# Kernel tuning notes

Hardware: AMD Instinct MI355X
Metric: run time of the kernel (lower is better)

## Reference

```python
import jax, jax.numpy as jnp
import numpy as np

N = 100_000
E = 1_600_000
IN_FT, HID, OUT = 512, 128, 64


def setup_inputs() -> dict:
    key = jax.random.key(0)
    ks = jax.random.split(key, 7)
    x = jax.random.normal(ks[0], (N, IN_FT), dtype=jnp.float32)
    edge_index = jax.random.randint(ks[1], (2, E), 0, N, dtype=jnp.int32)
    edge_weight = jax.random.uniform(ks[2], (E,), dtype=jnp.float32)
    W1 = jax.random.normal(ks[3], (IN_FT, HID), dtype=jnp.float32) * 0.05
    b1 = jnp.zeros((HID,), dtype=jnp.float32)
    W2 = jax.random.normal(ks[4], (HID, OUT), dtype=jnp.float32) * 0.05
    b2 = jnp.zeros((OUT,), dtype=jnp.float32)
    return {"x": x, "edge_index": edge_index, "edge_weight": edge_weight,
            "W1": W1, "b1": b1, "W2": W2, "b2": b2}


def reference(x, edge_index, edge_weight, W1, b1, W2, b2):
    n = x.shape[0]
    row, col = edge_index[0], edge_index[1]
    # PyG gcn_norm: add self-loops with weight 1, symmetric normalization
    loop = jnp.arange(n, dtype=row.dtype)
    r = jnp.concatenate([row, loop])
    c = jnp.concatenate([col, loop])
    w = jnp.concatenate([edge_weight, jnp.ones((n,), edge_weight.dtype)])
    deg = jax.ops.segment_sum(w, c, num_segments=n)
    dinv = jnp.where(deg > 0, jax.lax.rsqrt(deg), 0.0)
    norm = dinv[r] * w * dinv[c]  # [E + N]

    def conv(h, W, b):
        h = h @ W                                  # [N, F_out]
        msg = norm[:, None] * h[r]                 # gather source nodes
        return jax.ops.segment_sum(msg, c, num_segments=n) + b

    h = jax.nn.relu(conv(x, W1, b1))
    # dropout: inference mode (training=False) -> identity
    out = conv(h, W2, b2)
    return jax.nn.log_softmax(out, axis=1)
```

## Files before the change

kernel.cpp:

```cpp
#include <hip/hip_runtime.h>
#include <hip/hip_fp16.h>


constexpr int NN  = 100000;
constexpr int NE  = 1600000;
constexpr int FIN = 512;
constexpr int FH  = 128;
constexpr int FO  = 64;
constexpr int CAP = 64;

constexpr int NBLK1 = 512;
constexpr int EPB   = NE / NBLK1;
constexpr int NBKT  = 196;
constexpr int BCAP  = 9728;
constexpr int NWT   = FIN * FH + FH * FO;

constexpr float WSCALE  = 32767.0f;
constexpr float IWSCALE = 1.0f / 32767.0f;

typedef _Float16 f16x8 __attribute__((ext_vector_type(8)));
typedef float    f32x4 __attribute__((ext_vector_type(4)));

union F16Frag { _Float16 f[8]; short4 s[2]; f16x8 v; };

__device__ __forceinline__ void gload16(const void* g, void* l) {
    __builtin_amdgcn_global_load_lds(
        (const __attribute__((address_space(1))) void*)g,
        (__attribute__((address_space(3))) void*)l,
        16, 0, 0);
}


__global__ __launch_bounds__(256) void k_pass1(const int* __restrict__ rowi,
                                               const int* __restrict__ coli,
                                               const float* __restrict__ ew,
                                               const float* __restrict__ W1,
                                               const float* __restrict__ W2,
                                               _Float16* __restrict__ w1t,
                                               _Float16* __restrict__ w2t,
                                               int* __restrict__ bcur,
                                               unsigned long long* __restrict__ binned) {
    __shared__ unsigned long long buf[EPB];
    __shared__ int hist[NBKT];
    __shared__ int curs[NBKT];
    const int t = threadIdx.x;
    {
        int i = blockIdx.x * 256 + t;
        if (i < FIN * FH) {
            int k = i >> 7, c = i & 127;
            w1t[c * FIN + k] = (_Float16)W1[i];
        } else if (i < NWT) {
            int j = i - FIN * FH;
            int k = j >> 6, c = j & 63;
            w2t[c * FH + k] = (_Float16)W2[j];
        }
    }
    const int base = blockIdx.x * EPB;
    for (int i = t; i < NBKT; i += 256) hist[i] = 0;
    __syncthreads();
    for (int i = t; i < EPB; i += 256) {
        int e = base + i;
        int c = coli[e];
        unsigned wq = __float2uint_rn(ew[e] * WSCALE);
        buf[i] = ((unsigned long long)(unsigned)c << 32)
               | (unsigned long long)((wq << 17) | (unsigned)rowi[e]);
        atomicAdd(&hist[c >> 9], 1);
    }
    __syncthreads();
    if (t < NBKT) curs[t] = atomicAdd(&bcur[t], hist[t]);
    __syncthreads();
    for (int i = t; i < EPB; i += 256) {
        unsigned long long v = buf[i];
        int b = (int)(v >> 41);
        int pos = atomicAdd(&curs[b], 1);
        if ((unsigned)pos < BCAP) binned[(size_t)b * BCAP + pos] = v;
    }
}


__global__ __launch_bounds__(256) void k_pass2(const int* __restrict__ bcur,
                                               const unsigned long long* __restrict__ binned,
                                               unsigned* __restrict__ pay,
                                               int* __restrict__ cursor,
                                               float* __restrict__ dinv) {
    __shared__ int   cnt[512];
    __shared__ float wsum[512];
    const int t = threadIdx.x, b = blockIdx.x;
    for (int i = t; i < 512; i += 256) { cnt[i] = 0; wsum[i] = 0.f; }
    __syncthreads();
    const int total = min(bcur[b], BCAP);
    const int nbase = b * 512;
    for (int i = t; i < total; i += 256) {
        unsigned long long v = binned[(size_t)b * BCAP + i];
        int c9 = (int)((v >> 32) & 511);
        unsigned lo = (unsigned)v;
        int pos = atomicAdd(&cnt[c9], 1);
        atomicAdd(&wsum[c9], (float)(lo >> 17) * IWSCALE);
        if (pos < CAP) pay[(size_t)(nbase + c9) * CAP + pos] = lo;
    }
    __syncthreads();
    for (int i = t; i < 512; i += 256) {
        int node = nbase + i;
        if (node < NN) {
            cursor[node] = cnt[i];
            dinv[node]   = rsqrtf(1.0f + wsum[i]);
        }
    }
}


__global__ __launch_bounds__(256) void k_gemm1(const float* __restrict__ X,
                                               const _Float16* __restrict__ w1t,
                                               _Float16* __restrict__ H1) {
    __shared__ __align__(16) float    Asf[128 * 64];
    __shared__ __align__(16) _Float16 Bs[128 * 64];
    const int tid = threadIdx.x;
    const int wid = tid >> 6, l = tid & 63;
    const int wr = wid >> 1, wc = wid & 1;
    const int l15 = l & 15, lg = l >> 4;
    const int brow = blockIdx.x * 128;

    f32x4 acc[4][4];
#pragma unroll
    for (int m = 0; m < 4; ++m)
#pragma unroll
        for (int n = 0; n < 4; ++n) acc[m][n] = (f32x4){0.f, 0.f, 0.f, 0.f};

    const int rA = wid * 32 + (l >> 4);
    const int sA = l & 15;
    const int rB = wid * 32 + (l >> 3);
    const int sB = l & 7;

    for (int k0 = 0; k0 < FIN; k0 += 64) {
#pragma unroll
        for (int j = 0; j < 8; ++j) {
            int r  = rA + j * 4;
            int sg = sA ^ (r & 15);
            gload16(&X[(size_t)min(brow + r, NN - 1) * FIN + k0 + sg * 4],
                    &Asf[wid * 2048 + j * 256]);
        }
#pragma unroll
        for (int j = 0; j < 4; ++j) {
            int r  = rB + j * 8;
            int sg = sB ^ (r & 7);
            gload16(&w1t[(size_t)r * FIN + k0 + sg * 8],
                    &Bs[wid * 2048 + j * 512]);
        }
        __syncthreads();
#pragma unroll
        for (int ks = 0; ks < 2; ++ks) {
            F16Frag au[4], bu[4];
#pragma unroll
            for (int m = 0; m < 4; ++m) {
                int row = wr * 64 + m * 16 + l15;
                int slo = ks * 8 + lg;
                float4 lo = *(const float4*)&Asf[row * 64 + ((slo       ^ (row & 15)) * 4)];
                float4 hi = *(const float4*)&Asf[row * 64 + (((slo + 4) ^ (row & 15)) * 4)];
                au[m].f[0] = (_Float16)lo.x; au[m].f[1] = (_Float16)lo.y;
                au[m].f[2] = (_Float16)lo.z; au[m].f[3] = (_Float16)lo.w;
                au[m].f[4] = (_Float16)hi.x; au[m].f[5] = (_Float16)hi.y;
                au[m].f[6] = (_Float16)hi.z; au[m].f[7] = (_Float16)hi.w;
            }
#pragma unroll
            for (int n = 0; n < 4; ++n) {
                int row = wc * 64 + n * 16 + l15;
                int sb  = ks * 4 + (lg >> 1);
                int wi  = (lg & 1) * 4;
                bu[n].s[0] = *(const short4*)&Bs[row * 64 + ((sb       ^ (row & 7)) * 8) + wi];
                bu[n].s[1] = *(const short4*)&Bs[row * 64 + (((sb + 2) ^ (row & 7)) * 8) + wi];
            }
#pragma unroll
            for (int m = 0; m < 4; ++m)
#pragma unroll
                for (int n = 0; n < 4; ++n)
                    acc[m][n] = __builtin_amdgcn_mfma_f32_16x16x32_f16(
                        au[m].v, bu[n].v, acc[m][n], 0, 0, 0);
        }
        __syncthreads();
    }
#pragma unroll
    for (int m = 0; m < 4; ++m)
#pragma unroll
        for (int n = 0; n < 4; ++n) {
            int gcol = wc * 64 + n * 16 + l15;
#pragma unroll
            for (int r4 = 0; r4 < 4; ++r4) {
                int gr = brow + wr * 64 + m * 16 + lg * 4 + r4;
                if (gr < NN) H1[(size_t)gr * FH + gcol] = (_Float16)acc[m][n][r4];
            }
        }
}


__global__ __launch_bounds__(256) void k_gemm2(const _Float16* __restrict__ H2,
                                               const _Float16* __restrict__ w2t,
                                               _Float16* __restrict__ H3) {
    __shared__ __align__(16) _Float16 As[64 * 128];
    __shared__ __align__(16) _Float16 Bs[64 * 128];
    const int tid  = threadIdx.x;
    const int brow = blockIdx.x * 64;
    const int wid = tid >> 6, l = tid & 63;
    const int wr = wid >> 1, wc = wid & 1;
    const int l15 = l & 15, lg = l >> 4;

    f32x4 acc[2][2];
#pragma unroll
    for (int m = 0; m < 2; ++m)
#pragma unroll
        for (int n = 0; n < 2; ++n) acc[m][n] = (f32x4){0.f, 0.f, 0.f, 0.f};

    {
        int ar = tid >> 2, part = tid & 3, grow = brow + ar;
#pragma unroll
        for (int j = 0; j < 4; ++j) {
            int slot = part * 4 + j;
            int4 v = make_int4(0, 0, 0, 0);
            if (grow < NN) v = *(const int4*)&H2[(size_t)grow * FH + slot * 8];
            *(int4*)&As[ar * 128 + ((slot ^ (ar & 15)) * 8)] = v;
            *(int4*)&Bs[ar * 128 + ((slot ^ (ar & 15)) * 8)] =
                *(const int4*)&w2t[ar * FH + slot * 8];
        }
    }
    __syncthreads();
#pragma unroll
    for (int ks = 0; ks < 4; ++ks) {
        F16Frag au[2], bu[2];
        int klo = ks * 32 + 4 * lg;
        int khi = klo + 16;
#pragma unroll
        for (int m = 0; m < 2; ++m) {
            int row = wr * 32 + m * 16 + l15;
            int sw  = row & 15;
            au[m].s[0] = *(const short4*)&As[row * 128 + (((klo >> 3) ^ sw) * 8) + (klo & 7)];
            au[m].s[1] = *(const short4*)&As[row * 128 + (((khi >> 3) ^ sw) * 8) + (khi & 7)];
        }
#pragma unroll
        for (int n = 0; n < 2; ++n) {
            int row = wc * 32 + n * 16 + l15;
            int sw  = row & 15;
            bu[n].s[0] = *(const short4*)&Bs[row * 128 + (((klo >> 3) ^ sw) * 8) + (klo & 7)];
            bu[n].s[1] = *(const short4*)&Bs[row * 128 + (((khi >> 3) ^ sw) * 8) + (khi & 7)];
        }
#pragma unroll
        for (int m = 0; m < 2; ++m)
#pragma unroll
            for (int n = 0; n < 2; ++n)
                acc[m][n] = __builtin_amdgcn_mfma_f32_16x16x32_f16(
                    au[m].v, bu[n].v, acc[m][n], 0, 0, 0);
    }
#pragma unroll
    for (int m = 0; m < 2; ++m)
#pragma unroll
        for (int n = 0; n < 2; ++n) {
            int gcol = wc * 32 + n * 16 + l15;
#pragma unroll
            for (int r4 = 0; r4 < 4; ++r4) {
                int gr = brow + wr * 32 + m * 16 + lg * 4 + r4;
                if (gr < NN) H3[(size_t)gr * FO + gcol] = (_Float16)acc[m][n][r4];
            }
        }
}


__global__ __launch_bounds__(256) void k_agg1(const int* __restrict__ cursor,
                                              const unsigned* __restrict__ pay,
                                              const float* __restrict__ dinv,
                                              const __half* __restrict__ H1,
                                              const float* __restrict__ b1,
                                              __half* __restrict__ H2) {
    int node = (blockIdx.x * 256 + threadIdx.x) >> 6;
    int lane = threadIdx.x & 63;
    if (node >= NN) return;
    const int f = lane * 2;
    float dc  = dinv[node];
    float dcs = dc * IWSCALE;
    float2 hc = __half22float2(*(const __half2*)&H1[(size_t)node * FH + f]);
    float a0x = dc * dc * hc.x, a0y = dc * dc * hc.y;
    float a1x = 0, a1y = 0, a2x = 0, a2y = 0, a3x = 0, a3y = 0;
    int cnt = min(max(cursor[node], 0), CAP);
    const unsigned* p = &pay[(size_t)node * CAP];
    int e = 0;
    for (; e + 8 <= cnt; e += 8) {
        uint4 pa = *(const uint4*)&p[e];
        uint4 pb = *(const uint4*)&p[e + 4];
        int s0 = pa.x & 0x1FFFF, s1 = pa.y & 0x1FFFF, s2 = pa.z & 0x1FFFF, s3 = pa.w & 0x1FFFF;
        int s4 = pb.x & 0x1FFFF, s5 = pb.y & 0x1FFFF, s6 = pb.z & 0x1FFFF, s7 = pb.w & 0x1FFFF;
        float w0 = (float)(pa.x >> 17) * dcs * dinv[s0];
        float w1 = (float)(pa.y >> 17) * dcs * dinv[s1];
        float w2 = (float)(pa.z >> 17) * dcs * dinv[s2];
        float w3 = (float)(pa.w >> 17) * dcs * dinv[s3];
        float w4 = (float)(pb.x >> 17) * dcs * dinv[s4];
        float w5 = (float)(pb.y >> 17) * dcs * dinv[s5];
        float w6 = (float)(pb.z >> 17) * dcs * dinv[s6];
        float w7 = (float)(pb.w >> 17) * dcs * dinv[s7];
        float2 g0 = __half22float2(*(const __half2*)&H1[(size_t)s0 * FH + f]);
        float2 g1 = __half22float2(*(const __half2*)&H1[(size_t)s1 * FH + f]);
        float2 g2 = __half22float2(*(const __half2*)&H1[(size_t)s2 * FH + f]);
        float2 g3 = __half22float2(*(const __half2*)&H1[(size_t)s3 * FH + f]);
        float2 g4 = __half22float2(*(const __half2*)&H1[(size_t)s4 * FH + f]);
        float2 g5 = __half22float2(*(const __half2*)&H1[(size_t)s5 * FH + f]);
        float2 g6 = __half22float2(*(const __half2*)&H1[(size_t)s6 * FH + f]);
        float2 g7 = __half22float2(*(const __half2*)&H1[(size_t)s7 * FH + f]);
        a0x += w0 * g0.x; a0y += w0 * g0.y;  a1x += w1 * g1.x; a1y += w1 * g1.y;
        a2x += w2 * g2.x; a2y += w2 * g2.y;  a3x += w3 * g3.x; a3y += w3 * g3.y;
        a0x += w4 * g4.x; a0y += w4 * g4.y;  a1x += w5 * g5.x; a1y += w5 * g5.y;
        a2x += w6 * g6.x; a2y += w6 * g6.y;  a3x += w7 * g7.x; a3y += w7 * g7.y;
    }
    for (; e < cnt; ++e) {
        unsigned v = p[e];
        int s = v & 0x1FFFF;
        float w = (float)(v >> 17) * dcs * dinv[s];
        float2 g = __half22float2(*(const __half2*)&H1[(size_t)s * FH + f]);
        a0x += w * g.x; a0y += w * g.y;
    }
    float vx = a0x + a1x + a2x + a3x + b1[f];
    float vy = a0y + a1y + a2y + a3y + b1[f + 1];
    vx = vx > 0.f ? vx : 0.f;
    vy = vy > 0.f ? vy : 0.f;
    *(__half2*)&H2[(size_t)node * FH + f] = __floats2half2_rn(vx, vy);
}


__global__ __launch_bounds__(256) void k_agg2(const int* __restrict__ cursor,
                                              const unsigned* __restrict__ pay,
                                              const float* __restrict__ dinv,
                                              const __half* __restrict__ H3,
                                              const float* __restrict__ b2,
                                              float* __restrict__ out) {
    int node = (blockIdx.x * 256 + threadIdx.x) >> 6;
    int lane = threadIdx.x & 63;
    if (node >= NN) return;
    float dc  = dinv[node];
    float dcs = dc * IWSCALE;
    float a0 = dc * dc * __half2float(H3[(size_t)node * FO + lane]);
    float a1 = 0, a2 = 0, a3 = 0;
    int cnt = min(max(cursor[node], 0), CAP);
    const unsigned* p = &pay[(size_t)node * CAP];
    int e = 0;
    for (; e + 8 <= cnt; e += 8) {
        uint4 pa = *(const uint4*)&p[e];
        uint4 pb = *(const uint4*)&p[e + 4];
        int s0 = pa.x & 0x1FFFF, s1 = pa.y & 0x1FFFF, s2 = pa.z & 0x1FFFF, s3 = pa.w & 0x1FFFF;
        int s4 = pb.x & 0x1FFFF, s5 = pb.y & 0x1FFFF, s6 = pb.z & 0x1FFFF, s7 = pb.w & 0x1FFFF;
        float w0 = (float)(pa.x >> 17) * dcs * dinv[s0];
        float w1 = (float)(pa.y >> 17) * dcs * dinv[s1];
        float w2 = (float)(pa.z >> 17) * dcs * dinv[s2];
        float w3 = (float)(pa.w >> 17) * dcs * dinv[s3];
        float w4 = (float)(pb.x >> 17) * dcs * dinv[s4];
        float w5 = (float)(pb.y >> 17) * dcs * dinv[s5];
        float w6 = (float)(pb.z >> 17) * dcs * dinv[s6];
        float w7 = (float)(pb.w >> 17) * dcs * dinv[s7];
        a0 += w0 * __half2float(H3[(size_t)s0 * FO + lane]);
        a1 += w1 * __half2float(H3[(size_t)s1 * FO + lane]);
        a2 += w2 * __half2float(H3[(size_t)s2 * FO + lane]);
        a3 += w3 * __half2float(H3[(size_t)s3 * FO + lane]);
        a0 += w4 * __half2float(H3[(size_t)s4 * FO + lane]);
        a1 += w5 * __half2float(H3[(size_t)s5 * FO + lane]);
        a2 += w6 * __half2float(H3[(size_t)s6 * FO + lane]);
        a3 += w7 * __half2float(H3[(size_t)s7 * FO + lane]);
    }
    for (; e < cnt; ++e) {
        unsigned v = p[e];
        int s = v & 0x1FFFF;
        float w = (float)(v >> 17) * dcs * dinv[s];
        a0 += w * __half2float(H3[(size_t)s * FO + lane]);
    }
    float v = a0 + a1 + a2 + a3 + b2[lane];
    float m = v;
#pragma unroll
    for (int s = 32; s; s >>= 1) m = fmaxf(m, __shfl_xor(m, s));
    float ex = expf(v - m);
    float sum = ex;
#pragma unroll
    for (int s = 32; s; s >>= 1) sum += __shfl_xor(sum, s);
    out[(size_t)node * FO + lane] = v - m - logf(sum);
}


extern "C" void kernel_launch(void* const* d_in, const int* in_sizes, int n_in,
                              void* d_out, int out_size, void* d_ws, size_t ws_size,
                              hipStream_t stream) {
    const float* x   = (const float*)d_in[0];
    const int*   ei  = (const int*)d_in[1];
    const int*   row = ei;
    const int*   col = ei + NE;
    const float* ew  = (const float*)d_in[2];
    const float* W1  = (const float*)d_in[3];
    const float* b1  = (const float*)d_in[4];
    const float* W2  = (const float*)d_in[5];
    const float* b2  = (const float*)d_in[6];
    float* out = (float*)d_out;

    int*       bcur   = (int*)d_ws;
    int*       cursor = bcur + 256;
    float*     dinv   = (float*)(cursor + 102400);
    _Float16*  w1t    = (_Float16*)(dinv + 102400);
    _Float16*  w2t    = w1t + FIN * FH;
    unsigned long long* binned = (unsigned long long*)(w2t + FH * FO);
    unsigned*  pay    = (unsigned*)(binned + (size_t)NBKT * BCAP);
    _Float16*  H1     = (_Float16*)(pay + (size_t)NN * CAP);
    _Float16*  H2     = H1 + (size_t)NN * FH;
    _Float16*  H3     = H2 + (size_t)NN * FH;

    hipMemsetAsync(bcur, 0, NBKT * sizeof(int), stream);
    k_pass1<<<NBLK1, 256, 0, stream>>>(row, col, ew, W1, W2, w1t, w2t, bcur, binned);
    k_pass2<<<NBKT, 256, 0, stream>>>(bcur, binned, pay, cursor, dinv);

    k_gemm1<<<(NN + 127) / 128, 256, 0, stream>>>(x, w1t, H1);
    k_agg1 <<<(NN * 64 + 255) / 256, 256, 0, stream>>>(cursor, pay, dinv,
                                                       (const __half*)H1, b1, (__half*)H2);
    k_gemm2<<<(NN + 63) / 64, 256, 0, stream>>>(H2, w2t, H3);
    k_agg2 <<<(NN * 64 + 255) / 256, 256, 0, stream>>>(cursor, pay, dinv,
                                                       (const __half*)H3, b2, out);
}
```

Baseline: 260.5 us.

## Merge edge binning into the first GEMM launch and fold memset into prep

The edge-binning pass and the first feature GEMM are merged into one launch. The extra blocks at the end of the grid do the binning, and the earlier blocks run the GEMM, with shared memory overlaid through a union. Weight conversion and zeroing of the bucket counters move into a small prep kernel, which replaces the memset. The aim is to overlap the memory-bound binning with the GEMM and to drop launch gaps. The cost is that every block now reserves the larger shared footprint (buf is 25KB versus 48KB for the GEMM, so 48KB), and the extra prep launch must finish first.

```diff
diff --git a/kernel.cpp b/kernel.cpp
--- a/kernel.cpp
+++ b/kernel.cpp
@@ -14,6 +14,7 @@
 constexpr int NBKT  = 196;
 constexpr int BCAP  = 9728;
 constexpr int NWT   = FIN * FH + FH * FO;
+constexpr int NG    = (NN + 127) / 128;
 
 constexpr float WSCALE  = 32767.0f;
 constexpr float IWSCALE = 1.0f / 32767.0f;
@@ -31,50 +32,146 @@
 }
 
 
-__global__ __launch_bounds__(256) void k_pass1(const int* __restrict__ rowi,
-                                               const int* __restrict__ coli,
-                                               const float* __restrict__ ew,
-                                               const float* __restrict__ W1,
-                                               const float* __restrict__ W2,
-                                               _Float16* __restrict__ w1t,
-                                               _Float16* __restrict__ w2t,
-                                               int* __restrict__ bcur,
-                                               unsigned long long* __restrict__ binned) {
-    __shared__ unsigned long long buf[EPB];
-    __shared__ int hist[NBKT];
-    __shared__ int curs[NBKT];
-    const int t = threadIdx.x;
-    {
-        int i = blockIdx.x * 256 + t;
-        if (i < FIN * FH) {
-            int k = i >> 7, c = i & 127;
-            w1t[c * FIN + k] = (_Float16)W1[i];
-        } else if (i < NWT) {
-            int j = i - FIN * FH;
-            int k = j >> 6, c = j & 63;
-            w2t[c * FH + k] = (_Float16)W2[j];
-        }
-    }
-    const int base = blockIdx.x * EPB;
-    for (int i = t; i < NBKT; i += 256) hist[i] = 0;
-    __syncthreads();
-    for (int i = t; i < EPB; i += 256) {
-        int e = base + i;
-        int c = coli[e];
-        unsigned wq = __float2uint_rn(ew[e] * WSCALE);
-        buf[i] = ((unsigned long long)(unsigned)c << 32)
-               | (unsigned long long)((wq << 17) | (unsigned)rowi[e]);
-        atomicAdd(&hist[c >> 9], 1);
-    }
-    __syncthreads();
-    if (t < NBKT) curs[t] = atomicAdd(&bcur[t], hist[t]);
-    __syncthreads();
-    for (int i = t; i < EPB; i += 256) {
-        unsigned long long v = buf[i];
-        int b = (int)(v >> 41);
-        int pos = atomicAdd(&curs[b], 1);
-        if ((unsigned)pos < BCAP) binned[(size_t)b * BCAP + pos] = v;
-    }
+__global__ __launch_bounds__(256) void k_prep(const float* __restrict__ W1,
+                                              const float* __restrict__ W2,
+                                              int* __restrict__ bcur,
+                                              _Float16* __restrict__ w1t,
+                                              _Float16* __restrict__ w2t) {
+    int i = blockIdx.x * 256 + threadIdx.x;
+    if (i < NBKT) bcur[i] = 0;
+    if (i < FIN * FH) {
+        int k = i >> 7, c = i & 127;
+        w1t[c * FIN + k] = (_Float16)W1[i];
+    } else if (i < NWT) {
+        int j = i - FIN * FH;
+        int k = j >> 6, c = j & 63;
+        w2t[c * FH + k] = (_Float16)W2[j];
+    }
+}
+
+
+union MegaShared {
+    struct {
+        float    Asf[128 * 64];
+        _Float16 Bs[128 * 64];
+    } g;
+    struct {
+        unsigned long long buf[EPB];
+        int hist[NBKT];
+        int curs[NBKT];
+    } b;
+};
+
+__global__ __launch_bounds__(256) void k_mega(const float* __restrict__ X,
+                                              const _Float16* __restrict__ w1t,
+                                              _Float16* __restrict__ H1,
+                                              const int* __restrict__ rowi,
+                                              const int* __restrict__ coli,
+                                              const float* __restrict__ ew,
+                                              int* __restrict__ bcur,
+                                              unsigned long long* __restrict__ binned) {
+    __shared__ MegaShared sm;
+    const int tid = threadIdx.x;
+
+    if (blockIdx.x >= NG) {
+        const int bb   = blockIdx.x - NG;
+        const int base = bb * EPB;
+        for (int i = tid; i < NBKT; i += 256) sm.b.hist[i] = 0;
+        __syncthreads();
+        for (int i = tid; i < EPB; i += 256) {
+            int e = base + i;
+            int c = coli[e];
+            unsigned wq = __float2uint_rn(ew[e] * WSCALE);
+            sm.b.buf[i] = ((unsigned long long)(unsigned)c << 32)
+                        | (unsigned long long)((wq << 17) | (unsigned)rowi[e]);
+            atomicAdd(&sm.b.hist[c >> 9], 1);
+        }
+        __syncthreads();
+        if (tid < NBKT) sm.b.curs[tid] = atomicAdd(&bcur[tid], sm.b.hist[tid]);
+        __syncthreads();
+        for (int i = tid; i < EPB; i += 256) {
+            unsigned long long v = sm.b.buf[i];
+            int b = (int)(v >> 41);
+            int pos = atomicAdd(&sm.b.curs[b], 1);
+            if ((unsigned)pos < BCAP) binned[(size_t)b * BCAP + pos] = v;
+        }
+        return;
+    }
+
+    const int wid = tid >> 6, l = tid & 63;
+    const int wr = wid >> 1, wc = wid & 1;
+    const int l15 = l & 15, lg = l >> 4;
+    const int brow = blockIdx.x * 128;
+
+    f32x4 acc[4][4];
+#pragma unroll
+    for (int m = 0; m < 4; ++m)
+#pragma unroll
+        for (int n = 0; n < 4; ++n) acc[m][n] = (f32x4){0.f, 0.f, 0.f, 0.f};
+
+    const int rA = wid * 32 + (l >> 4);
+    const int sA = l & 15;
+    const int rB = wid * 32 + (l >> 3);
+    const int sB = l & 7;
+
+    for (int k0 = 0; k0 < FIN; k0 += 64) {
+#pragma unroll
+        for (int j = 0; j < 8; ++j) {
+            int r  = rA + j * 4;
+            int sg = sA ^ (r & 15);
+            gload16(&X[(size_t)min(brow + r, NN - 1) * FIN + k0 + sg * 4],
+                    &sm.g.Asf[wid * 2048 + j * 256]);
+        }
+#pragma unroll
+        for (int j = 0; j < 4; ++j) {
+            int r  = rB + j * 8;
+            int sg = sB ^ (r & 7);
+            gload16(&w1t[(size_t)r * FIN + k0 + sg * 8],
+                    &sm.g.Bs[wid * 2048 + j * 512]);
+        }
+        __syncthreads();
+#pragma unroll
+        for (int ks = 0; ks < 2; ++ks) {
+            F16Frag au[4], bu[4];
+#pragma unroll
+            for (int m = 0; m < 4; ++m) {
+                int row = wr * 64 + m * 16 + l15;
+                int slo = ks * 8 + lg;
+                float4 lo = *(const float4*)&sm.g.Asf[row * 64 + ((slo       ^ (row & 15)) * 4)];
+                float4 hi = *(const float4*)&sm.g.Asf[row * 64 + (((slo + 4) ^ (row & 15)) * 4)];
+                au[m].f[0] = (_Float16)lo.x; au[m].f[1] = (_Float16)lo.y;
+                au[m].f[2] = (_Float16)lo.z; au[m].f[3] = (_Float16)lo.w;
+                au[m].f[4] = (_Float16)hi.x; au[m].f[5] = (_Float16)hi.y;
+                au[m].f[6] = (_Float16)hi.z; au[m].f[7] = (_Float16)hi.w;
+            }
+#pragma unroll
+            for (int n = 0; n < 4; ++n) {
+                int row = wc * 64 + n * 16 + l15;
+                int sb  = ks * 4 + (lg >> 1);
+                int wi  = (lg & 1) * 4;
+                bu[n].s[0] = *(const short4*)&sm.g.Bs[row * 64 + ((sb       ^ (row & 7)) * 8) + wi];
+                bu[n].s[1] = *(const short4*)&sm.g.Bs[row * 64 + (((sb + 2) ^ (row & 7)) * 8) + wi];
+            }
+#pragma unroll
+            for (int m = 0; m < 4; ++m)
+#pragma unroll
+                for (int n = 0; n < 4; ++n)
+                    acc[m][n] = __builtin_amdgcn_mfma_f32_16x16x32_f16(
+                        au[m].v, bu[n].v, acc[m][n], 0, 0, 0);
+        }
+        __syncthreads();
+    }
+#pragma unroll
+    for (int m = 0; m < 4; ++m)
+#pragma unroll
+        for (int n = 0; n < 4; ++n) {
+            int gcol = wc * 64 + n * 16 + l15;
+#pragma unroll
+            for (int r4 = 0; r4 < 4; ++r4) {
+                int gr = brow + wr * 64 + m * 16 + lg * 4 + r4;
+                if (gr < NN) H1[(size_t)gr * FH + gcol] = (_Float16)acc[m][n][r4];
+            }
+        }
 }
 
 
@@ -106,89 +203,6 @@
             dinv[node]   = rsqrtf(1.0f + wsum[i]);
         }
     }
-}
-
-
-__global__ __launch_bounds__(256) void k_gemm1(const float* __restrict__ X,
-                                               const _Float16* __restrict__ w1t,
-                                               _Float16* __restrict__ H1) {
-    __shared__ __align__(16) float    Asf[128 * 64];
-    __shared__ __align__(16) _Float16 Bs[128 * 64];
-    const int tid = threadIdx.x;
-    const int wid = tid >> 6, l = tid & 63;
-    const int wr = wid >> 1, wc = wid & 1;
-    const int l15 = l & 15, lg = l >> 4;
-    const int brow = blockIdx.x * 128;
-
-    f32x4 acc[4][4];
-#pragma unroll
-    for (int m = 0; m < 4; ++m)
-#pragma unroll
-        for (int n = 0; n < 4; ++n) acc[m][n] = (f32x4){0.f, 0.f, 0.f, 0.f};
-
-    const int rA = wid * 32 + (l >> 4);
-    const int sA = l & 15;
-    const int rB = wid * 32 + (l >> 3);
-    const int sB = l & 7;
-
-    for (int k0 = 0; k0 < FIN; k0 += 64) {
-#pragma unroll
-        for (int j = 0; j < 8; ++j) {
-            int r  = rA + j * 4;
-            int sg = sA ^ (r & 15);
-            gload16(&X[(size_t)min(brow + r, NN - 1) * FIN + k0 + sg * 4],
-                    &Asf[wid * 2048 + j * 256]);
-        }
-#pragma unroll
-        for (int j = 0; j < 4; ++j) {
-            int r  = rB + j * 8;
-            int sg = sB ^ (r & 7);
-            gload16(&w1t[(size_t)r * FIN + k0 + sg * 8],
-                    &Bs[wid * 2048 + j * 512]);
-        }
-        __syncthreads();
-#pragma unroll
-        for (int ks = 0; ks < 2; ++ks) {
-            F16Frag au[4], bu[4];
-#pragma unroll
-            for (int m = 0; m < 4; ++m) {
-                int row = wr * 64 + m * 16 + l15;
-                int slo = ks * 8 + lg;
-                float4 lo = *(const float4*)&Asf[row * 64 + ((slo       ^ (row & 15)) * 4)];
-                float4 hi = *(const float4*)&Asf[row * 64 + (((slo + 4) ^ (row & 15)) * 4)];
-                au[m].f[0] = (_Float16)lo.x; au[m].f[1] = (_Float16)lo.y;
-                au[m].f[2] = (_Float16)lo.z; au[m].f[3] = (_Float16)lo.w;
-                au[m].f[4] = (_Float16)hi.x; au[m].f[5] = (_Float16)hi.y;
-                au[m].f[6] = (_Float16)hi.z; au[m].f[7] = (_Float16)hi.w;
-            }
-#pragma unroll
-            for (int n = 0; n < 4; ++n) {
-                int row = wc * 64 + n * 16 + l15;
-                int sb  = ks * 4 + (lg >> 1);
-                int wi  = (lg & 1) * 4;
-                bu[n].s[0] = *(const short4*)&Bs[row * 64 + ((sb       ^ (row & 7)) * 8) + wi];
-                bu[n].s[1] = *(const short4*)&Bs[row * 64 + (((sb + 2) ^ (row & 7)) * 8) + wi];
-            }
-#pragma unroll
-            for (int m = 0; m < 4; ++m)
-#pragma unroll
-                for (int n = 0; n < 4; ++n)
-                    acc[m][n] = __builtin_amdgcn_mfma_f32_16x16x32_f16(
-                        au[m].v, bu[n].v, acc[m][n], 0, 0, 0);
-        }
-        __syncthreads();
-    }
-#pragma unroll
-    for (int m = 0; m < 4; ++m)
-#pragma unroll
-        for (int n = 0; n < 4; ++n) {
-            int gcol = wc * 64 + n * 16 + l15;
-#pragma unroll
-            for (int r4 = 0; r4 < 4; ++r4) {
-                int gr = brow + wr * 64 + m * 16 + lg * 4 + r4;
-                if (gr < NN) H1[(size_t)gr * FH + gcol] = (_Float16)acc[m][n][r4];
-            }
-        }
 }
 
 
@@ -402,11 +416,10 @@
     _Float16*  H2     = H1 + (size_t)NN * FH;
     _Float16*  H3     = H2 + (size_t)NN * FH;
 
-    hipMemsetAsync(bcur, 0, NBKT * sizeof(int), stream);
-    k_pass1<<<NBLK1, 256, 0, stream>>>(row, col, ew, W1, W2, w1t, w2t, bcur, binned);
+    k_prep <<<(NWT + 255) / 256, 256, 0, stream>>>(W1, W2, bcur, w1t, w2t);
+    k_mega <<<NG + NBLK1, 256, 0, stream>>>(x, w1t, H1, row, col, ew, bcur, binned);
     k_pass2<<<NBKT, 256, 0, stream>>>(bcur, binned, pay, cursor, dinv);
 
-    k_gemm1<<<(NN + 127) / 128, 256, 0, stream>>>(x, w1t, H1);
     k_agg1 <<<(NN * 64 + 255) / 256, 256, 0, stream>>>(cursor, pay, dinv,
                                                        (const __half*)H1, b1, (__half*)H2);
     k_gemm2<<<(NN + 63) / 64, 256, 0, stream>>>(H2, w2t, H3);
```

After: 251.6 us (median of 2 runs). 3.4% less time.
